# Optimization experiments

Hardware: AMD Instinct MI355X
Metric: run time of the kernel (lower is better)

## Reference

```python
import jax, jax.numpy as jnp
import numpy as np
from jax import lax

B, C, H, W = 32, 128, 56, 56
SIZE = C * H * W
EPS = 1e-5
SLOPE = 0.1


def setup_inputs() -> dict:
    key = jax.random.key(0)
    ks = jax.random.split(key, 12)
    return {
        "ax": jax.random.normal(ks[0], (B, C, H, W), dtype=jnp.float32),
        "mx": jax.random.normal(ks[1], (B, C, H, W), dtype=jnp.float32),
        # grouped conv1d (groups=SIZE, k=2, no bias) == per-position pair weights [SIZE, 2]
        "cfc_w": jax.random.normal(ks[2], (SIZE, 2), dtype=jnp.float32) * 0.1,
        # BatchNorm1d (eval mode) params over SIZE channels
        "bn_gamma": jax.random.normal(ks[3], (SIZE,), dtype=jnp.float32) * 0.1 + 1.0,
        "bn_beta": jax.random.normal(ks[4], (SIZE,), dtype=jnp.float32) * 0.1,
        "bn_mean": jax.random.normal(ks[5], (SIZE,), dtype=jnp.float32) * 0.1,
        "bn_var": jax.random.uniform(ks[6], (SIZE,), dtype=jnp.float32, minval=0.5, maxval=1.5),
        # conv3x3, C->C, bias
        "conv_w": jax.random.normal(ks[7], (C, C, 3, 3), dtype=jnp.float32) * (1.0 / np.sqrt(C * 9)),
        "conv_b": jax.random.normal(ks[8], (C,), dtype=jnp.float32) * 0.01,
        # BatchNorm2d (eval mode) params over C channels
        "bn2_gamma": jax.random.normal(ks[9], (C,), dtype=jnp.float32) * 0.1 + 1.0,
        "bn2_beta": jax.random.normal(ks[10], (C,), dtype=jnp.float32) * 0.1,
        "bn2_mean": jax.random.normal(ks[11], (C,), dtype=jnp.float32) * 0.1,
        "bn2_var": jax.random.uniform(jax.random.fold_in(key, 99), (C,), dtype=jnp.float32, minval=0.5, maxval=1.5),
    }


def reference(ax, mx, cfc_w, bn_gamma, bn_beta, bn_mean, bn_var,
              conv_w, conv_b, bn2_gamma, bn2_beta, bn2_mean, bn2_var):
    b, c, h, w = ax.shape
    a = ax.reshape(b, -1)  # [B, SIZE]
    m = mx.reshape(b, -1)
    # degenerate grouped Conv1d(k=2, groups=SIZE): z_i = w_i0 * a_i + w_i1 * m_i
    z = cfc_w[:, 0] * a + cfc_w[:, 1] * m
    # BatchNorm1d (eval) + LeakyReLU(0.1)
    z = (z - bn_mean) * (bn_gamma / jnp.sqrt(bn_var + EPS)) + bn_beta
    z = jax.nn.leaky_relu(z, SLOPE).reshape(b, c, h, w)
    # conv3x3 (stride 1, pad 1) + bias
    y = lax.conv_general_dilated(z, conv_w, window_strides=(1, 1),
                                 padding=((1, 1), (1, 1)),
                                 dimension_numbers=("NCHW", "OIHW", "NCHW"))
    y = y + conv_b[None, :, None, None]
    # BatchNorm2d (eval) + LeakyReLU(0.1)
    scale = (bn2_gamma / jnp.sqrt(bn2_var + EPS))[None, :, None, None]
    y = (y - bn2_mean[None, :, None, None]) * scale + bn2_beta[None, :, None, None]
    return jax.nn.leaky_relu(y, SLOPE)
```

## Files before the change

### kernel.cpp

```cpp
#include <hip/hip_runtime.h>

#define B_ 32
#define C_ 128
#define H_ 56
#define W_ 56
#define HW_ (H_*W_)
#define SIZE_ (C_*HW_)
#define NPIX_ (B_*HW_)
#define HP_ 58
#define WP_ 58
#define PLANE_ (HP_*WP_*C_)
#define K_ 1152
#define EPS_ 1e-5f
#define SLOPE_ 0.1f

typedef __bf16 bf16x8 __attribute__((ext_vector_type(8)));
typedef float  f32x4  __attribute__((ext_vector_type(4)));

__device__ __forceinline__ ushort f2bf(float x) {
    union { float f; unsigned u; } v; v.f = x;
    return (ushort)((v.u + 0x7FFFu + ((v.u >> 16) & 1u)) >> 16);
}
__device__ __forceinline__ float lrelu(float z) { return z > 0.f ? z : SLOPE_ * z; }

__device__ __forceinline__ void glds16(const ushort* g, ushort* l) {
    __builtin_amdgcn_global_load_lds(
        (const __attribute__((address_space(1))) unsigned int*)g,
        (__attribute__((address_space(3))) unsigned int*)l, 16, 0, 0);
}

__global__ __launch_bounds__(256) void prep_kernel(
    const float* __restrict__ conv_w, const float* __restrict__ conv_b,
    const float* __restrict__ g2, const float* __restrict__ b2,
    const float* __restrict__ m2, const float* __restrict__ v2,
    const float2* __restrict__ cfc, const float* __restrict__ g1,
    const float* __restrict__ b1, const float* __restrict__ mu1,
    const float* __restrict__ v1,
    ushort* __restrict__ wA, float* __restrict__ scale2, float* __restrict__ shift2,
    float* __restrict__ p0, float* __restrict__ p1, float* __restrict__ p2)
{
    int tid = blockIdx.x * 256 + threadIdx.x;
    if (tid < C_ * K_) {
        int co = tid / K_;
        int k  = tid - co * K_;
        int khkw = k >> 7, ci = k & 127;
        int kh = khkw / 3, kw = khkw - 3 * kh;
        wA[tid] = f2bf(conv_w[((co * C_ + ci) * 3 + kh) * 3 + kw]);
    }
    if (tid < C_) {
        float sc = g2[tid] * rsqrtf(v2[tid] + EPS_);
        scale2[tid] = sc;
        shift2[tid] = (conv_b[tid] - m2[tid]) * sc + b2[tid];
    }
    if (tid < SIZE_) {
        float sc = g1[tid] * rsqrtf(v1[tid] + EPS_);
        float2 wv = cfc[tid];
        p0[tid] = wv.x * sc;
        p1[tid] = wv.y * sc;
        p2[tid] = b1[tid] - mu1[tid] * sc;
    }
}

__global__ __launch_bounds__(256) void zfuse_kernel(
    const float4* __restrict__ ax, const float4* __restrict__ mx,
    const float4* __restrict__ p0, const float4* __restrict__ p1,
    const float4* __restrict__ p2, ushort* __restrict__ zp)
{
    __shared__ ushort tile[C_ * 58];
    const int hp = blockIdx.x, b = blockIdx.y;
    const int tid = threadIdx.x;
    ushort* row = zp + (size_t)b * PLANE_ + (size_t)hp * (WP_ * C_);
    if (hp == 0 || hp == HP_ - 1) {
        uint2* r2 = (uint2*)row;
        for (int i = tid; i < WP_ * C_ / 4; i += 256) r2[i] = make_uint2(0u, 0u);
        return;
    }
    const int h = hp - 1;
    const int base4 = (b * SIZE_) >> 2;
    for (int i = tid; i < 1792; i += 256) {
        int c  = i / 14;
        int w4 = i - c * 14;
        int s4 = c * (HW_ / 4) + h * (W_ / 4) + w4;
        float4 a = ax[base4 + s4];
        float4 m = mx[base4 + s4];
        float4 q0 = p0[s4], q1 = p1[s4], q2 = p2[s4];
        uint z0 = f2bf(lrelu(a.x * q0.x + m.x * q1.x + q2.x));
        uint z1 = f2bf(lrelu(a.y * q0.y + m.y * q1.y + q2.y));
        uint z2 = f2bf(lrelu(a.z * q0.z + m.z * q1.z + q2.z));
        uint z3 = f2bf(lrelu(a.w * q0.w + m.w * q1.w + q2.w));
        uint* t32 = (uint*)(tile + c * 58 + w4 * 4);
        t32[0] = z0 | (z1 << 16);
        t32[1] = z2 | (z3 << 16);
    }
    __syncthreads();
    if (tid < 64) {
        int side = tid >> 5, cc = tid & 31;
        *(uint2*)(row + side * (57 * C_) + cc * 4) = make_uint2(0u, 0u);
    }
    for (int j = tid; j < 1792; j += 256) {
        int w  = j >> 5;
        int c0 = (j & 31) * 4;
        uint lo = (uint)tile[(c0 + 0) * 58 + w] | ((uint)tile[(c0 + 1) * 58 + w] << 16);
        uint hi = (uint)tile[(c0 + 2) * 58 + w] | ((uint)tile[(c0 + 3) * 58 + w] << 16);
        *(uint2*)(row + (w + 1) * C_ + c0) = make_uint2(lo, hi);
    }
}

__global__ __launch_bounds__(256) void conv_kernel(
    const ushort* __restrict__ zp, const ushort* __restrict__ wA,
    const float* __restrict__ scale2, const float* __restrict__ shift2,
    float* __restrict__ out)
{
    __shared__ ushort As[2 * 4096];
    __shared__ ushort Bs[2 * 4096];

    const int tid  = threadIdx.x;
    const int wave = tid >> 6, lane = tid & 63;
    const int l16  = lane & 15, quad = lane >> 4;
    const int blk  = blockIdx.x;
    const int pbase = ((blk & 7) * 98 + (blk >> 3)) * 128;

    const int srow = wave * 32 + (lane >> 2);
    const int sch  = (lane & 3) ^ ((lane >> 3) & 3);
    const ushort* agA0 = wA + srow * K_ + sch * 8;

    int pf0 = pbase + srow;
    int bb0 = pf0 / HW_, pi0 = pf0 - bb0 * HW_;
    int h0 = pi0 / W_, w0 = pi0 - h0 * W_;
    const ushort* bgB0 = zp + (size_t)bb0 * PLANE_ + (h0 * WP_ + w0) * C_ + sch * 8;
    int pf1 = pf0 + 16;
    int bb1 = pf1 / HW_, pi1 = pf1 - bb1 * HW_;
    int h1 = pi1 / W_, w1 = pi1 - h1 * W_;
    const ushort* bgB1 = zp + (size_t)bb1 * PLANE_ + (h1 * WP_ + w1) * C_ + sch * 8;

    ushort* aD = As + wave * 1024;
    ushort* bD = Bs + wave * 1024;

    auto stage = [&](int s, int buf) {
        int tap = s >> 2;
        int ko  = (s & 3) * 32;
        int kh  = tap / 3, kw = tap - 3 * kh;
        int aoff = tap * C_ + ko;
        int boff = (kh * WP_ + kw) * C_ + ko;
        glds16(agA0 + aoff,           aD + buf * 4096);
        glds16(agA0 + 16 * K_ + aoff, aD + buf * 4096 + 512);
        glds16(bgB0 + boff,           bD + buf * 4096);
        glds16(bgB1 + boff,           bD + buf * 4096 + 512);
    };

    const int cob = (wave & 1) * 64;
    const int pxb = (wave >> 1) * 64;
    const int swq = (quad ^ ((l16 >> 1) & 3)) * 8;

    f32x4 acc[4][4] = {};
    stage(0, 0);
    #pragma unroll 2
    for (int s = 0; s < 36; ++s) {
        const int cur = s & 1;
        __syncthreads();
        if (s < 35) stage(s + 1, cur ^ 1);
        const ushort* Ab = As + cur * 4096;
        const ushort* Bb = Bs + cur * 4096;
        bf16x8 af[4], bfr[4];
        #pragma unroll
        for (int mt = 0; mt < 4; ++mt)
            af[mt] = *(const bf16x8*)(Ab + (cob + mt * 16 + l16) * 32 + swq);
        #pragma unroll
        for (int nt = 0; nt < 4; ++nt)
            bfr[nt] = *(const bf16x8*)(Bb + (pxb + nt * 16 + l16) * 32 + swq);
        #pragma unroll
        for (int mt = 0; mt < 4; ++mt)
            #pragma unroll
            for (int nt = 0; nt < 4; ++nt)
                acc[mt][nt] = __builtin_amdgcn_mfma_f32_16x16x32_bf16(
                    af[mt], bfr[nt], acc[mt][nt], 0, 0, 0);
    }

    int pob[4];
    #pragma unroll
    for (int nt = 0; nt < 4; ++nt) {
        int pf = pbase + pxb + nt * 16 + l16;
        int bb = pf / HW_;
        pob[nt] = bb * SIZE_ + (pf - bb * HW_);
    }
    #pragma unroll
    for (int mt = 0; mt < 4; ++mt) {
        #pragma unroll
        for (int r = 0; r < 4; ++r) {
            int co = cob + mt * 16 + quad * 4 + r;
            float sc = scale2[co], sh = shift2[co];
            #pragma unroll
            for (int nt = 0; nt < 4; ++nt) {
                float v = acc[mt][nt][r] * sc + sh;
                out[(size_t)pob[nt] + co * HW_] = lrelu(v);
            }
        }
    }
}

extern "C" void kernel_launch(void* const* d_in, const int* in_sizes, int n_in,
                              void* d_out, int out_size, void* d_ws, size_t ws_size,
                              hipStream_t stream) {
    const float* ax     = (const float*)d_in[0];
    const float* mx     = (const float*)d_in[1];
    const float* cfc    = (const float*)d_in[2];
    const float* bn_g   = (const float*)d_in[3];
    const float* bn_b   = (const float*)d_in[4];
    const float* bn_m   = (const float*)d_in[5];
    const float* bn_v   = (const float*)d_in[6];
    const float* conv_w = (const float*)d_in[7];
    const float* conv_b = (const float*)d_in[8];
    const float* g2     = (const float*)d_in[9];
    const float* b2     = (const float*)d_in[10];
    const float* m2     = (const float*)d_in[11];
    const float* v2     = (const float*)d_in[12];
    float* out = (float*)d_out;

    char* ws = (char*)d_ws;
    ushort* zp     = (ushort*)ws;
    ushort* wA     = (ushort*)(ws + 27557888);
    float*  scale2 = (float*)(ws + 27852800);
    float*  shift2 = (float*)(ws + 27853312);
    float*  p0     = (float*)(ws + 27853824);
    float*  p1     = (float*)(ws + 29459456);
    float*  p2     = (float*)(ws + 31065088);

    prep_kernel<<<dim3((SIZE_ + 255) / 256), 256, 0, stream>>>(
        conv_w, conv_b, g2, b2, m2, v2, (const float2*)cfc,
        bn_g, bn_b, bn_m, bn_v, wA, scale2, shift2, p0, p1, p2);
    zfuse_kernel<<<dim3(HP_, B_), 256, 0, stream>>>(
        (const float4*)ax, (const float4*)mx,
        (const float4*)p0, (const float4*)p1, (const float4*)p2, zp);
    conv_kernel<<<dim3(NPIX_ / 128), 256, 0, stream>>>(zp, wA, scale2, shift2, out);
}
```

Baseline: 237.9 us.

## Drop LDS staging in conv; load MFMA fragments directly from global memory

Removes the double-buffered LDS pipeline (global_load_lds plus barriers) from the implicit-GEMM conv kernel. Each wave now loads its bf16 A and B fragments straight from global memory into registers. The weights are pre-permuted into a k-slab-major layout so each fragment read is contiguous. This drops the per-step __syncthreads and LDS traffic, but the two waves sharing each operand now both read it from global/L2, and there is no explicit prefetch to hide load latency behind the MFMAs.

After: 283.1 us. 1.19x slower.

```diff
diff --git a/kernel.cpp b/kernel.cpp
--- a/kernel.cpp
+++ b/kernel.cpp
@@ -23,12 +23,6 @@
 }
 __device__ __forceinline__ float lrelu(float z) { return z > 0.f ? z : SLOPE_ * z; }
 
-__device__ __forceinline__ void glds16(const ushort* g, ushort* l) {
-    __builtin_amdgcn_global_load_lds(
-        (const __attribute__((address_space(1))) unsigned int*)g,
-        (__attribute__((address_space(3))) unsigned int*)l, 16, 0, 0);
-}
-
 __global__ __launch_bounds__(256) void prep_kernel(
     const float* __restrict__ conv_w, const float* __restrict__ conv_b,
     const float* __restrict__ g2, const float* __restrict__ b2,
@@ -36,7 +30,7 @@
     const float2* __restrict__ cfc, const float* __restrict__ g1,
     const float* __restrict__ b1, const float* __restrict__ mu1,
     const float* __restrict__ v1,
-    ushort* __restrict__ wA, float* __restrict__ scale2, float* __restrict__ shift2,
+    ushort* __restrict__ wAf, float* __restrict__ scale2, float* __restrict__ shift2,
     float* __restrict__ p0, float* __restrict__ p1, float* __restrict__ p2)
 {
     int tid = blockIdx.x * 256 + threadIdx.x;
@@ -45,7 +39,8 @@
         int k  = tid - co * K_;
         int khkw = k >> 7, ci = k & 127;
         int kh = khkw / 3, kw = khkw - 3 * kh;
-        wA[tid] = f2bf(conv_w[((co * C_ + ci) * 3 + kh) * 3 + kw]);
+        float v = conv_w[((co * C_ + ci) * 3 + kh) * 3 + kw];
+        wAf[(k >> 5) * 4096 + co * 32 + (k & 31)] = f2bf(v);
     }
     if (tid < C_) {
         float sc = g2[tid] * rsqrtf(v2[tid] + EPS_);
@@ -107,73 +102,54 @@
 }
 
 __global__ __launch_bounds__(256) void conv_kernel(
-    const ushort* __restrict__ zp, const ushort* __restrict__ wA,
+    const ushort* __restrict__ zp, const ushort* __restrict__ wAf,
     const float* __restrict__ scale2, const float* __restrict__ shift2,
     float* __restrict__ out)
 {
-    __shared__ ushort As[2 * 4096];
-    __shared__ ushort Bs[2 * 4096];
-
     const int tid  = threadIdx.x;
     const int wave = tid >> 6, lane = tid & 63;
     const int l16  = lane & 15, quad = lane >> 4;
     const int blk  = blockIdx.x;
     const int pbase = ((blk & 7) * 98 + (blk >> 3)) * 128;
 
-    const int srow = wave * 32 + (lane >> 2);
-    const int sch  = (lane & 3) ^ ((lane >> 3) & 3);
-    const ushort* agA0 = wA + srow * K_ + sch * 8;
-
-    int pf0 = pbase + srow;
-    int bb0 = pf0 / HW_, pi0 = pf0 - bb0 * HW_;
-    int h0 = pi0 / W_, w0 = pi0 - h0 * W_;
-    const ushort* bgB0 = zp + (size_t)bb0 * PLANE_ + (h0 * WP_ + w0) * C_ + sch * 8;
-    int pf1 = pf0 + 16;
-    int bb1 = pf1 / HW_, pi1 = pf1 - bb1 * HW_;
-    int h1 = pi1 / W_, w1 = pi1 - h1 * W_;
-    const ushort* bgB1 = zp + (size_t)bb1 * PLANE_ + (h1 * WP_ + w1) * C_ + sch * 8;
-
-    ushort* aD = As + wave * 1024;
-    ushort* bD = Bs + wave * 1024;
-
-    auto stage = [&](int s, int buf) {
-        int tap = s >> 2;
-        int ko  = (s & 3) * 32;
-        int kh  = tap / 3, kw = tap - 3 * kh;
-        int aoff = tap * C_ + ko;
-        int boff = (kh * WP_ + kw) * C_ + ko;
-        glds16(agA0 + aoff,           aD + buf * 4096);
-        glds16(agA0 + 16 * K_ + aoff, aD + buf * 4096 + 512);
-        glds16(bgB0 + boff,           bD + buf * 4096);
-        glds16(bgB1 + boff,           bD + buf * 4096 + 512);
-    };
-
     const int cob = (wave & 1) * 64;
     const int pxb = (wave >> 1) * 64;
-    const int swq = (quad ^ ((l16 >> 1) & 3)) * 8;
+
+    const ushort* bp[4];
+    #pragma unroll
+    for (int nt = 0; nt < 4; ++nt) {
+        int p  = pbase + pxb + nt * 16 + l16;
+        int bb = p / HW_, pi = p - bb * HW_;
+        int h = pi / W_, w = pi - h * W_;
+        bp[nt] = zp + (size_t)bb * PLANE_ + (h * WP_ + w) * C_ + quad * 8;
+    }
+    const ushort* ap = wAf + (cob + l16) * 32 + quad * 8;
 
     f32x4 acc[4][4] = {};
-    stage(0, 0);
-    #pragma unroll 2
-    for (int s = 0; s < 36; ++s) {
-        const int cur = s & 1;
-        __syncthreads();
-        if (s < 35) stage(s + 1, cur ^ 1);
-        const ushort* Ab = As + cur * 4096;
-        const ushort* Bb = Bs + cur * 4096;
-        bf16x8 af[4], bfr[4];
+
+    #pragma unroll
+    for (int tap = 0; tap < 9; ++tap) {
+        const int kh = tap / 3, kw = tap - 3 * kh;
+        const int boff = (kh * WP_ + kw) * C_;
         #pragma unroll
-        for (int mt = 0; mt < 4; ++mt)
-            af[mt] = *(const bf16x8*)(Ab + (cob + mt * 16 + l16) * 32 + swq);
-        #pragma unroll
-        for (int nt = 0; nt < 4; ++nt)
-            bfr[nt] = *(const bf16x8*)(Bb + (pxb + nt * 16 + l16) * 32 + swq);
-        #pragma unroll
-        for (int mt = 0; mt < 4; ++mt)
+        for (int ks = 0; ks < 4; ++ks) {
+            const int s  = tap * 4 + ks;
+            const int ao = s * 4096;
+            const int bo = boff + ks * 32;
+            bf16x8 af[4], bfr[4];
+            #pragma unroll
+            for (int mt = 0; mt < 4; ++mt)
+                af[mt] = *(const bf16x8*)(ap + ao + mt * 512);
             #pragma unroll
             for (int nt = 0; nt < 4; ++nt)
-                acc[mt][nt] = __builtin_amdgcn_mfma_f32_16x16x32_bf16(
-                    af[mt], bfr[nt], acc[mt][nt], 0, 0, 0);
+                bfr[nt] = *(const bf16x8*)(bp[nt] + bo);
+            #pragma unroll
+            for (int mt = 0; mt < 4; ++mt)
+                #pragma unroll
+                for (int nt = 0; nt < 4; ++nt)
+                    acc[mt][nt] = __builtin_amdgcn_mfma_f32_16x16x32_bf16(
+                        af[mt], bfr[nt], acc[mt][nt], 0, 0, 0);
+        }
     }
 
     int pob[4];
@@ -218,7 +194,7 @@
 
     char* ws = (char*)d_ws;
     ushort* zp     = (ushort*)ws;
-    ushort* wA     = (ushort*)(ws + 27557888);
+    ushort* wAf    = (ushort*)(ws + 27557888);
     float*  scale2 = (float*)(ws + 27852800);
     float*  shift2 = (float*)(ws + 27853312);
     float*  p0     = (float*)(ws + 27853824);
@@ -227,9 +203,9 @@
 
     prep_kernel<<<dim3((SIZE_ + 255) / 256), 256, 0, stream>>>(
         conv_w, conv_b, g2, b2, m2, v2, (const float2*)cfc,
-        bn_g, bn_b, bn_m, bn_v, wA, scale2, shift2, p0, p1, p2);
+        bn_g, bn_b, bn_m, bn_v, wAf, scale2, shift2, p0, p1, p2);
     zfuse_kernel<<<dim3(HP_, B_), 256, 0, stream>>>(
         (const float4*)ax, (const float4*)mx,
         (const float4*)p0, (const float4*)p1, (const float4*)p2, zp);
-    conv_kernel<<<dim3(NPIX_ / 128), 256, 0, stream>>>(zp, wA, scale2, shift2, out);
-}
+    conv_kernel<<<dim3(NPIX_ / 128), 256, 0, stream>>>(zp, wAf, scale2, shift2, out);
+}
```

## Stage conv tiles through registers with two-deep prefetch instead of direct-to-LDS loads

Applied to the files above, without the earlier changes.

Replaces the global_load_lds direct-to-LDS staging in the implicit-GEMM conv loop with ordinary vector global loads into registers, issued two k-steps ahead and written to the alternate LDS buffer after the MFMAs. The loop is also fully unrolled, and the barrier moves to the end of each iteration. The aim is to hide global latency behind more compute and let the compiler schedule loads and MFMAs freely. In exchange it uses more VGPRs for the in-flight register buffers and adds explicit LDS write instructions.

After: 402.2 us. 1.69x slower.

```diff
diff --git a/kernel.cpp b/kernel.cpp
--- a/kernel.cpp
+++ b/kernel.cpp
@@ -22,12 +22,6 @@
     return (ushort)((v.u + 0x7FFFu + ((v.u >> 16) & 1u)) >> 16);
 }
 __device__ __forceinline__ float lrelu(float z) { return z > 0.f ? z : SLOPE_ * z; }
-
-__device__ __forceinline__ void glds16(const ushort* g, ushort* l) {
-    __builtin_amdgcn_global_load_lds(
-        (const __attribute__((address_space(1))) unsigned int*)g,
-        (__attribute__((address_space(3))) unsigned int*)l, 16, 0, 0);
-}
 
 __global__ __launch_bounds__(256) void prep_kernel(
     const float* __restrict__ conv_w, const float* __restrict__ conv_b,
@@ -133,32 +127,42 @@
     int h1 = pi1 / W_, w1 = pi1 - h1 * W_;
     const ushort* bgB1 = zp + (size_t)bb1 * PLANE_ + (h1 * WP_ + w1) * C_ + sch * 8;
 
-    ushort* aD = As + wave * 1024;
-    ushort* bD = Bs + wave * 1024;
-
-    auto stage = [&](int s, int buf) {
-        int tap = s >> 2;
-        int ko  = (s & 3) * 32;
-        int kh  = tap / 3, kw = tap - 3 * kh;
-        int aoff = tap * C_ + ko;
-        int boff = (kh * WP_ + kw) * C_ + ko;
-        glds16(agA0 + aoff,           aD + buf * 4096);
-        glds16(agA0 + 16 * K_ + aoff, aD + buf * 4096 + 512);
-        glds16(bgB0 + boff,           bD + buf * 4096);
-        glds16(bgB1 + boff,           bD + buf * 4096 + 512);
-    };
+    ushort* aW = As + wave * 1024 + lane * 8;
+    ushort* bW = Bs + wave * 1024 + lane * 8;
 
     const int cob = (wave & 1) * 64;
     const int pxb = (wave >> 1) * 64;
     const int swq = (quad ^ ((l16 >> 1) & 3)) * 8;
 
+    uint4 ra[2][2], rb[2][2];
+
+    auto loadst = [&](int s, int t) {
+        int tap = s >> 2, ko = (s & 3) * 32;
+        int kh = tap / 3, kw = tap - 3 * kh;
+        int aoff = tap * C_ + ko;
+        int boff = (kh * WP_ + kw) * C_ + ko;
+        ra[t][0] = *(const uint4*)(agA0 + aoff);
+        ra[t][1] = *(const uint4*)(agA0 + 16 * K_ + aoff);
+        rb[t][0] = *(const uint4*)(bgB0 + boff);
+        rb[t][1] = *(const uint4*)(bgB1 + boff);
+    };
+    auto writest = [&](int buf, int t) {
+        *(uint4*)(aW + buf * 4096)       = ra[t][0];
+        *(uint4*)(aW + buf * 4096 + 512) = ra[t][1];
+        *(uint4*)(bW + buf * 4096)       = rb[t][0];
+        *(uint4*)(bW + buf * 4096 + 512) = rb[t][1];
+    };
+
     f32x4 acc[4][4] = {};
-    stage(0, 0);
-    #pragma unroll 2
+    loadst(0, 0);
+    loadst(1, 1);
+    writest(0, 0);
+    __syncthreads();
+
+    #pragma unroll
     for (int s = 0; s < 36; ++s) {
         const int cur = s & 1;
-        __syncthreads();
-        if (s < 35) stage(s + 1, cur ^ 1);
+        if (s + 2 < 36) loadst(s + 2, cur);
         const ushort* Ab = As + cur * 4096;
         const ushort* Bb = Bs + cur * 4096;
         bf16x8 af[4], bfr[4];
@@ -174,6 +178,8 @@
             for (int nt = 0; nt < 4; ++nt)
                 acc[mt][nt] = __builtin_amdgcn_mfma_f32_16x16x32_bf16(
                     af[mt], bfr[nt], acc[mt][nt], 0, 0, 0);
+        if (s + 1 < 36) writest(cur ^ 1, cur ^ 1);
+        __syncthreads();
     }
 
     int pob[4];
```
